# Performance work log

Measured on AMD Instinct MI355X. Metric: run time of the kernel, lower is better.

The kernel has to match this reference:

```python
import jax, jax.numpy as jnp
import numpy as np

D_MODEL = 96
D_INNER = 192   # ssm_ratio * d_model
R = 6           # dt_rank = ceil(96/16)
DH = 32         # d_inner // dt_rank (per-head dim)
K = 4           # scan directions
N = 16          # d_state
EPS = 1e-5


def setup_inputs() -> dict:
    key = jax.random.key(0)
    ks = jax.random.split(key, 10)
    B, H, W = 8, 64, 64
    f = lambda k, s, sc: jax.random.normal(k, s, jnp.float32) * sc
    return dict(
        x=jax.random.normal(ks[0], (B, H, W, D_MODEL), jnp.float32),
        w_in=f(ks[1], (D_MODEL, D_INNER), 0.02),
        w_conv=f(ks[2], (3, 3, 1, D_INNER), 0.1),      # depthwise HWIO
        b_conv=f(ks[3], (D_INNER,), 0.1),
        x_proj_weight=f(ks[4], (K, R + 2 * N, D_INNER), 0.02),
        A_logs=f(ks[5], (K, R), 0.5),
        Ds=jnp.ones((K, R, DH), jnp.float32),
        dt_bias=0.1 * jax.random.uniform(ks[6], (K, R), jnp.float32),
        ln_g=jnp.ones((D_INNER,), jnp.float32),
        ln_b=jnp.zeros((D_INNER,), jnp.float32),
        w_out=f(ks[7], (D_INNER, D_MODEL), 0.02),
    )


def _cross_scan(x):
    # x: (B,H,W,C) -> (B,L,4,C): [row-major, col-major, rev row, rev col]
    B, H, W, C = x.shape
    x0 = x.reshape(B, H * W, C)
    x1 = jnp.transpose(x, (0, 2, 1, 3)).reshape(B, H * W, C)
    return jnp.stack([x0, x1, x0[:, ::-1], x1[:, ::-1]], axis=2)


def _cross_merge(ys, H, W):
    # ys: (B,L,4,C) -> (B,L,C) summed after undoing each scan order
    B, L, _, C = ys.shape
    y_row = ys[:, :, 0] + ys[:, :, 2][:, ::-1]
    y_col = ys[:, :, 1] + ys[:, :, 3][:, ::-1]
    y_col = jnp.transpose(y_col.reshape(B, W, H, C), (0, 2, 1, 3)).reshape(B, L, C)
    return y_row + y_col


def _selective_scan(us, dts, As, Bs, Cs, Dsr, dtb):
    # us:(B,L,KR,DH) dts:(B,L,KR) As:(KR,) Bs,Cs:(B,L,K,N) Dsr:(KR,DH) dtb:(KR,)
    dt = jax.nn.softplus(dts + dtb)                 # (B,L,KR)
    decay = jnp.exp(dt * As)                        # (B,L,KR)
    xu = dt[..., None] * us                         # (B,L,KR,DH)
    Bh = jnp.repeat(Bs, R, axis=2)                  # (B,L,KR,N) head h -> group h//R
    Ch = jnp.repeat(Cs, R, axis=2)
    B_, L, KR, _ = us.shape
    tfirst = lambda a: jnp.moveaxis(a, 1, 0)

    def step(h, inp):
        dec, xu_t, b_t, c_t = inp                   # (B,KR),(B,KR,DH),(B,KR,N),(B,KR,N)
        h = dec[:, :, None, None] * h + xu_t[..., None] * b_t[:, :, None, :]
        y = jnp.einsum('bkdn,bkn->bkd', h, c_t)
        return h, y

    h0 = jnp.zeros((B_, KR, DH, N), us.dtype)
    _, ys = jax.lax.scan(step, h0, (tfirst(decay), tfirst(xu), tfirst(Bh), tfirst(Ch)))
    ys = jnp.moveaxis(ys, 0, 1)                     # (B,L,KR,DH)
    return ys + us * Dsr                            # skip term D*u


def reference(x, w_in, w_conv, b_conv, x_proj_weight, A_logs, Ds, dt_bias, ln_g, ln_b, w_out):
    B, H, W, _ = x.shape
    L = H * W
    xi = x @ w_in                                   # in_proj (no bias)
    xi = jax.lax.conv_general_dilated(
        xi, w_conv, (1, 1), 'SAME', feature_group_count=D_INNER,
        dimension_numbers=('NHWC', 'HWIO', 'NHWC')) + b_conv
    xi = jax.nn.silu(xi)
    xs = _cross_scan(xi)                            # (B,L,4,D_INNER)
    x_dbl = jnp.einsum('blkd,kcd->blkc', xs, x_proj_weight)
    dts = x_dbl[..., :R].reshape(B, L, K * R)
    Bs = x_dbl[..., R:R + N]                        # (B,L,K,N)
    Cs = x_dbl[..., R + N:]
    us = xs.reshape(B, L, K * R, DH)
    As = -jnp.exp(A_logs.astype(jnp.float32)).reshape(K * R)
    Dsr = Ds.reshape(K * R, DH)
    dtb = dt_bias.reshape(K * R)
    ys = _selective_scan(us, dts, As, Bs, Cs, Dsr, dtb)   # (B,L,KR,DH)
    y = _cross_merge(ys.reshape(B, L, K, R * DH), H, W)   # (B,L,D_INNER)
    mu = y.mean(-1, keepdims=True)
    var = ((y - mu) ** 2).mean(-1, keepdims=True)
    y = (y - mu) / jnp.sqrt(var + EPS) * ln_g + ln_b
    y = y.reshape(B, H, W, D_INNER)
    return y @ w_out                                # out_proj (no bias)
```

## Files before the change

### kernel.cpp

```cpp
#include <hip/hip_runtime.h>
#include <hip/hip_bf16.h>

#define BB 8
#define LL 4096
#define DM 96
#define DI 192
#define RRR 6
#define DHH 32
#define KKK 4
#define NNN 16
#define KRR 24
#define NCH 64
#define TT 64
#define RST 48

typedef unsigned short u16;
typedef __attribute__((ext_vector_type(8))) __bf16 bf16x8;
typedef __attribute__((ext_vector_type(4))) float f32x4;

__device__ __forceinline__ float softplus_f(float x){
    float ax = fabsf(x);
    return fmaxf(x, 0.f) + __logf(1.f + __expf(-ax));
}
__device__ __forceinline__ float silu_f(float x){ return x / (1.f + __expf(-x)); }

__device__ __forceinline__ void split_bf16(float v, u16& h, u16& l){
    __bf16 hb = (__bf16)v;
    h = __builtin_bit_cast(u16, hb);
    float r = v - (float)hb;
    l = __builtin_bit_cast(u16, (__bf16)r);
}

__global__ void k0p(const float* __restrict__ W, const float* __restrict__ g,
                    const float* __restrict__ bta, const float* __restrict__ w_out,
                    u16* __restrict__ WhB, u16* __restrict__ WlB,
                    float* __restrict__ wg, float* __restrict__ sgbw){
    int i = blockIdx.x * 256 + threadIdx.x;
    if (i < 2 * 80 * 192){
        int k = i % 192; int n80 = i / 192; int z = n80 / 80; int n = n80 % 80;
        int sub = n / 40, nc = n % 40;
        int dir = (z == 0) ? (sub ? 2 : 0) : (sub ? 3 : 1);
        float v = 0.f;
        if (nc < 6) v = W[(dir * 38 + nc) * DI + k];
        else if (nc >= 8) v = W[(dir * 38 + (nc - 2)) * DI + k];
        u16 h, l; split_bf16(v, h, l);
        WhB[i] = h; WlB[i] = l;
    } else if (i < 30720 + DI * DM){
        int j = i - 30720; int c = j / DM;
        wg[j] = w_out[j] * g[c];
    } else if (i < 30720 + DI * DM + DM){
        int m = i - (30720 + DI * DM);
        float s = 0.f, t = 0.f;
        for (int c = 0; c < DI; ++c){
            float w = w_out[c * DM + m];
            s = fmaf(g[c], w, s);
            t = fmaf(bta[c], w, t);
        }
        sgbw[m] = s; sgbw[DM + m] = t;
    }
}

__global__ __launch_bounds__(384) void k1_inproj(const float* __restrict__ x,
                                                 const float* __restrict__ w_in,
                                                 float* __restrict__ xw){
    __shared__ float xT[DM][36];
    int pix0 = blockIdx.x * 32;
    for (int i = threadIdx.x; i < 32 * 24; i += 384){
        int c4 = i % 24, p = i / 24;
        float4 v = *(const float4*)(x + (size_t)(pix0 + p) * DM + c4 * 4);
        xT[c4 * 4 + 0][p] = v.x; xT[c4 * 4 + 1][p] = v.y;
        xT[c4 * 4 + 2][p] = v.z; xT[c4 * 4 + 3][p] = v.w;
    }
    __syncthreads();
    int cg = threadIdx.x % 48, pg = threadIdx.x / 48;
    int p0 = pg * 4;
    float4 acc[4];
    #pragma unroll
    for (int i = 0; i < 4; ++i) acc[i] = make_float4(0.f, 0.f, 0.f, 0.f);
    const float* wcol = w_in + cg * 4;
    for (int d0 = 0; d0 < DM; d0 += 8){
        float4 wv[8], xv[8];
        #pragma unroll
        for (int j = 0; j < 8; ++j){
            wv[j] = *(const float4*)(wcol + (d0 + j) * DI);
            xv[j] = *(const float4*)(&xT[d0 + j][p0]);
        }
        #pragma unroll
        for (int j = 0; j < 8; ++j){
            float xs[4] = {xv[j].x, xv[j].y, xv[j].z, xv[j].w};
            #pragma unroll
            for (int pi = 0; pi < 4; ++pi){
                acc[pi].x = fmaf(xs[pi], wv[j].x, acc[pi].x);
                acc[pi].y = fmaf(xs[pi], wv[j].y, acc[pi].y);
                acc[pi].z = fmaf(xs[pi], wv[j].z, acc[pi].z);
                acc[pi].w = fmaf(xs[pi], wv[j].w, acc[pi].w);
            }
        }
    }
    #pragma unroll
    for (int pi = 0; pi < 4; ++pi)
        *(float4*)(xw + (size_t)(pix0 + p0 + pi) * DI + cg * 4) = acc[pi];
}

__global__ void k2_conv(const float* __restrict__ xw, const float* __restrict__ wc,
                        const float* __restrict__ bc, float* __restrict__ xi,
                        float* __restrict__ xiT){
    int gid = blockIdx.x * 256 + threadIdx.x;
    int c4 = gid % 48; int pix = gid / 48;
    int b = pix >> 12; int l = pix & 4095; int h = l >> 6; int w = l & 63;
    int c = c4 * 4;
    float4 acc = *(const float4*)(bc + c);
    #pragma unroll
    for (int dh = 0; dh < 3; ++dh){
        int hh = h + dh - 1; if ((unsigned)hh >= 64u) continue;
        #pragma unroll
        for (int dw = 0; dw < 3; ++dw){
            int ww2 = w + dw - 1; if ((unsigned)ww2 >= 64u) continue;
            float4 tap = *(const float4*)(xw + (size_t)((b << 12) + (hh << 6) + ww2) * DI + c);
            float4 wv  = *(const float4*)(wc + (dh * 3 + dw) * DI + c);
            acc.x = fmaf(tap.x, wv.x, acc.x);
            acc.y = fmaf(tap.y, wv.y, acc.y);
            acc.z = fmaf(tap.z, wv.z, acc.z);
            acc.w = fmaf(tap.w, wv.w, acc.w);
        }
    }
    acc.x = silu_f(acc.x); acc.y = silu_f(acc.y); acc.z = silu_f(acc.z); acc.w = silu_f(acc.w);
    *(float4*)(xi + (size_t)pix * DI + c) = acc;
    int lT = ((l & 63) << 6) | (l >> 6);
    *(float4*)(xiT + (size_t)((b << 12) + lT) * DI + c) = acc;
}

__global__ __launch_bounds__(256) void k3seq(const float* __restrict__ xi,
                                             const float* __restrict__ xiT,
                                             const u16* __restrict__ WhB,
                                             const u16* __restrict__ WlB,
                                             const float* __restrict__ A_logs,
                                             const float* __restrict__ dtb,
                                             float* __restrict__ rec){
    __shared__ u16 Xh[64][104];
    __shared__ u16 Xl[64][104];
    int z = blockIdx.y, b = blockIdx.z;
    int l0 = blockIdx.x * 64;
    const float* src = (z ? xiT : xi) + ((((size_t)b) << 12) + l0) * DI;
    int wv = threadIdx.x >> 6, lane = threadIdx.x & 63;
    int quad = lane >> 4, mi = lane & 15;
    int m0 = wv * 16;
    f32x4 acc[5];
    #pragma unroll
    for (int nt = 0; nt < 5; ++nt) acc[nt] = (f32x4){0.f, 0.f, 0.f, 0.f};
    const u16* wh = WhB + (size_t)z * 80 * 192;
    const u16* wl = WlB + (size_t)z * 80 * 192;
    #pragma unroll
    for (int half = 0; half < 2; ++half){
        __syncthreads();
        for (int i = threadIdx.x; i < 1536; i += 256){
            int c4 = i % 24, p = i / 24;
            float4 v = *(const float4*)(src + (size_t)p * DI + half * 96 + c4 * 4);
            u16 h0, h1, h2, h3, q0, q1, q2, q3;
            split_bf16(v.x, h0, q0); split_bf16(v.y, h1, q1);
            split_bf16(v.z, h2, q2); split_bf16(v.w, h3, q3);
            *(ushort4*)&Xh[p][c4 * 4] = make_ushort4(h0, h1, h2, h3);
            *(ushort4*)&Xl[p][c4 * 4] = make_ushort4(q0, q1, q2, q3);
        }
        __syncthreads();
        #pragma unroll
        for (int kt = 0; kt < 3; ++kt){
            int ko = kt * 32 + quad * 8;
            bf16x8 ah = *(const bf16x8*)&Xh[m0 + mi][ko];
            bf16x8 al = *(const bf16x8*)&Xl[m0 + mi][ko];
            int kg = half * 96 + ko;
            #pragma unroll
            for (int nt = 0; nt < 5; ++nt){
                const size_t woff = (size_t)(nt * 16 + mi) * 192 + kg;
                bf16x8 bh = *(const bf16x8*)(wh + woff);
                bf16x8 bl = *(const bf16x8*)(wl + woff);
                acc[nt] = __builtin_amdgcn_mfma_f32_16x16x32_bf16(ah, bh, acc[nt], 0, 0, 0);
                acc[nt] = __builtin_amdgcn_mfma_f32_16x16x32_bf16(al, bh, acc[nt], 0, 0, 0);
                acc[nt] = __builtin_amdgcn_mfma_f32_16x16x32_bf16(ah, bl, acc[nt], 0, 0, 0);
            }
        }
    }
    #pragma unroll
    for (int nt = 0; nt < 5; ++nt){
        int nc = nt * 16 + mi;
        int sub = nc / 40;
        int dir = (z == 0) ? (sub ? 2 : 0) : (sub ? 3 : 1);
        int c40 = nc % 40;
        float* rb = rec + (size_t)(b * KKK + dir) * LL * RST;
        bool isdt = (c40 < 6);
        bool ispad = (c40 == 6) | (c40 == 7);
        float Ac = 0.f, bc = 0.f;
        if (isdt){ Ac = -__expf(A_logs[dir * RRR + c40]); bc = dtb[dir * RRR + c40]; }
        #pragma unroll
        for (int i = 0; i < 4; ++i){
            int l = l0 + m0 + quad * 4 + i;
            int t = (sub == 0) ? l : (LL - 1 - l);
            float v = acc[nt][i];
            float* rw = rb + (size_t)t * RST;
            if (isdt){
                float dt = softplus_f(v + bc);
                rw[c40] = dt;
                rw[c40 + 8] = __expf(dt * Ac);
            } else if (!ispad){
                rw[c40 + 8] = v;
            }
        }
    }
}

__global__ __launch_bounds__(192) void k4a(const float* __restrict__ xi, const float* __restrict__ xiT,
                                           const float* __restrict__ rec, const float* __restrict__ Ds,
                                           float* __restrict__ Pb, float* __restrict__ Sb,
                                           float* __restrict__ pp, __hip_bfloat16* __restrict__ ybuf){
    int chunk = blockIdx.x, k = blockIdx.y, b = blockIdx.z;
    int r = threadIdx.x >> 5, d = threadIdx.x & 31;
    int kr = k * RRR + r;
    float Dv = Ds[kr * DHH + d];
    const float* rp = rec + ((size_t)(b * KKK + k) * LL + chunk * TT) * RST;
    const float* xb = ((k & 1) ? xiT : xi) + (((size_t)b) << 12) * DI + r * DHH + d;
    const float* up; ptrdiff_t ust;
    if (k < 2){ up = xb + (size_t)(chunk * TT) * DI;          ust = DI;  }
    else      { up = xb + (size_t)(LL - 1 - chunk * TT) * DI; ust = -(ptrdiff_t)DI; }
    __hip_bfloat16* yp = ybuf + ((size_t)(k * BB + b) * LL + chunk * TT) * DI + r * DHH + d;
    float* ppp = pp + ((size_t)(b * KKK + k) * RRR + r) * LL + chunk * TT;
    float h[NNN];
    #pragma unroll
    for (int n = 0; n < NNN; ++n) h[n] = 0.f;
    float ppv = 1.f;
    #pragma unroll 2
    for (int tt = 0; tt < TT; ++tt){
        float dt  = rp[r];
        float dec = rp[8 + r];
        float u = *up;
        float xu = dt * u;
        ppv *= dec;
        float Bv[NNN], Cv[NNN];
        *(float4*)(Bv + 0)  = *(const float4*)(rp + 16);
        *(float4*)(Bv + 4)  = *(const float4*)(rp + 20);
        *(float4*)(Bv + 8)  = *(const float4*)(rp + 24);
        *(float4*)(Bv + 12) = *(const float4*)(rp + 28);
        *(float4*)(Cv + 0)  = *(const float4*)(rp + 32);
        *(float4*)(Cv + 4)  = *(const float4*)(rp + 36);
        *(float4*)(Cv + 8)  = *(const float4*)(rp + 40);
        *(float4*)(Cv + 12) = *(const float4*)(rp + 44);
        float y = 0.f;
        #pragma unroll
        for (int n = 0; n < NNN; ++n){
            h[n] = fmaf(dec, h[n], xu * Bv[n]);
            y = fmaf(h[n], Cv[n], y);
        }
        y = fmaf(u, Dv, y);
        *yp = __float2bfloat16(y);
        if (d == 0) ppp[tt] = ppv;
        rp += RST; up += ust; yp += DI;
    }
    size_t sb = (((size_t)(b * KRR + kr) * NCH + chunk) * DHH + d) * NNN;
    #pragma unroll
    for (int n = 0; n < NNN; ++n) Sb[sb + n] = h[n];
    if (d == 0) Pb[(size_t)(b * KRR + kr) * NCH + chunk] = ppv;
}

__global__ __launch_bounds__(256) void k4b(const float* __restrict__ Pb, float* __restrict__ Sb){
    int scan = blockIdx.x >> 1;
    int half = blockIdx.x & 1;
    int tid = half * 256 + threadIdx.x;
    size_t base = (size_t)scan * NCH * 512 + tid;
    const float* Pp = Pb + (size_t)scan * NCH;
    float s[NCH];
    #pragma unroll
    for (int c = 0; c < NCH; ++c) s[c] = Sb[base + (size_t)c * 512];
    float hb = 0.f;
    #pragma unroll
    for (int c = 0; c < NCH; ++c){
        float nv = fmaf(Pp[c], hb, s[c]);
        Sb[base + (size_t)c * 512] = hb;
        hb = nv;
    }
}

__global__ __launch_bounds__(192) void k4corr(const float* __restrict__ rec,
                                              const float* __restrict__ Sb,
                                              const float* __restrict__ pp,
                                              __hip_bfloat16* __restrict__ ybuf){
    int chunk = blockIdx.x + 1;
    int k = blockIdx.y, b = blockIdx.z;
    int r = threadIdx.x >> 5, d = threadIdx.x & 31;
    int kr = k * RRR + r;
    float hi[NNN];
    size_t sb = (((size_t)(b * KRR + kr) * NCH + chunk) * DHH + d) * NNN;
    #pragma unroll
    for (int n = 0; n < NNN; ++n) hi[n] = Sb[sb + n];
    const float* rp = rec + ((size_t)(b * KKK + k) * LL + chunk * TT) * RST + 32;
    const float* ppp = pp + ((size_t)(b * KKK + k) * RRR + r) * LL + chunk * TT;
    __hip_bfloat16* yp = ybuf + ((size_t)(k * BB + b) * LL + chunk * TT) * DI + r * DHH + d;
    #pragma unroll 4
    for (int tt = 0; tt < TT; ++tt){
        float Cv[NNN];
        *(float4*)(Cv + 0)  = *(const float4*)(rp + 0);
        *(float4*)(Cv + 4)  = *(const float4*)(rp + 4);
        *(float4*)(Cv + 8)  = *(const float4*)(rp + 8);
        *(float4*)(Cv + 12) = *(const float4*)(rp + 12);
        float dv = 0.f;
        #pragma unroll
        for (int n = 0; n < NNN; ++n) dv = fmaf(hi[n], Cv[n], dv);
        float y = __bfloat162float(*yp);
        y = fmaf(ppp[tt], dv, y);
        *yp = __float2bfloat16(y);
        rp += RST; yp += DI;
    }
}

__global__ __launch_bounds__(256) void k5_out(const __hip_bfloat16* __restrict__ ybuf,
                       const float* __restrict__ wg, const float* __restrict__ sgbw,
                       float* __restrict__ out){
    __shared__ float yT[DI][36];
    __shared__ float rsL[32], rmL[32];
    int pix0 = blockIdx.x * 32;
    int b = pix0 >> 12;
    int l0 = pix0 & 4095;
    const __hip_bfloat16* y0 = ybuf + (size_t)(0 * BB + b) * LL * DI;
    const __hip_bfloat16* y1 = ybuf + (size_t)(1 * BB + b) * LL * DI;
    const __hip_bfloat16* y2 = ybuf + (size_t)(2 * BB + b) * LL * DI;
    const __hip_bfloat16* y3 = ybuf + (size_t)(3 * BB + b) * LL * DI;
    for (int i = threadIdx.x; i < 32 * DI; i += 256){
        int c = i % DI, p = i / DI;
        int l = l0 + p; int hh = l >> 6, ww = l & 63;
        int lT = (ww << 6) | hh;
        float s = __bfloat162float(y0[(size_t)l * DI + c])
                + __bfloat162float(y2[(size_t)(LL - 1 - l) * DI + c])
                + __bfloat162float(y1[(size_t)lT * DI + c])
                + __bfloat162float(y3[(size_t)(LL - 1 - lT) * DI + c]);
        yT[c][p] = s;
    }
    __syncthreads();
    {
        int p = threadIdx.x >> 3, cg = threadIdx.x & 7;
        float s = 0.f, s2 = 0.f;
        for (int c = cg; c < DI; c += 8){ float v = yT[c][p]; s += v; s2 = fmaf(v, v, s2); }
        s += __shfl_xor(s, 1, 64); s2 += __shfl_xor(s2, 1, 64);
        s += __shfl_xor(s, 2, 64); s2 += __shfl_xor(s2, 2, 64);
        s += __shfl_xor(s, 4, 64); s2 += __shfl_xor(s2, 4, 64);
        if (cg == 0){
            float mu = s * (1.f / DI);
            float var = s2 * (1.f / DI) - mu * mu;
            float rs = rsqrtf(var + 1e-5f);
            rsL[p] = rs; rmL[p] = rs * mu;
        }
    }
    __syncthreads();
    if (threadIdx.x < 192){
        int mg = threadIdx.x % 24, pg = threadIdx.x / 24;
        int p0 = pg * 4;
        float4 acc[4];
        #pragma unroll
        for (int i = 0; i < 4; ++i) acc[i] = make_float4(0.f, 0.f, 0.f, 0.f);
        const float* wcol = wg + mg * 4;
        for (int c0 = 0; c0 < DI; c0 += 8){
            float4 wv[8], yv[8];
            #pragma unroll
            for (int j = 0; j < 8; ++j){
                wv[j] = *(const float4*)(wcol + (c0 + j) * DM);
                yv[j] = *(const float4*)(&yT[c0 + j][p0]);
            }
            #pragma unroll
            for (int j = 0; j < 8; ++j){
                float ys[4] = {yv[j].x, yv[j].y, yv[j].z, yv[j].w};
                #pragma unroll
                for (int pi = 0; pi < 4; ++pi){
                    acc[pi].x = fmaf(ys[pi], wv[j].x, acc[pi].x);
                    acc[pi].y = fmaf(ys[pi], wv[j].y, acc[pi].y);
                    acc[pi].z = fmaf(ys[pi], wv[j].z, acc[pi].z);
                    acc[pi].w = fmaf(ys[pi], wv[j].w, acc[pi].w);
                }
            }
        }
        float4 sg4 = *(const float4*)(sgbw + mg * 4);
        float4 bw4 = *(const float4*)(sgbw + DM + mg * 4);
        #pragma unroll
        for (int pi = 0; pi < 4; ++pi){
            float rs = rsL[p0 + pi], rm = rmL[p0 + pi];
            float4 o;
            o.x = fmaf(acc[pi].x, rs, fmaf(-rm, sg4.x, bw4.x));
            o.y = fmaf(acc[pi].y, rs, fmaf(-rm, sg4.y, bw4.y));
            o.z = fmaf(acc[pi].z, rs, fmaf(-rm, sg4.z, bw4.z));
            o.w = fmaf(acc[pi].w, rs, fmaf(-rm, sg4.w, bw4.w));
            *(float4*)(out + (size_t)(pix0 + p0 + pi) * DM + mg * 4) = o;
        }
    }
}

extern "C" void kernel_launch(void* const* d_in, const int* in_sizes, int n_in,
                              void* d_out, int out_size, void* d_ws, size_t ws_size,
                              hipStream_t stream){
    const float* x      = (const float*)d_in[0];
    const float* w_in   = (const float*)d_in[1];
    const float* w_conv = (const float*)d_in[2];
    const float* b_conv = (const float*)d_in[3];
    const float* xproj  = (const float*)d_in[4];
    const float* A_logs = (const float*)d_in[5];
    const float* Ds     = (const float*)d_in[6];
    const float* dtbias = (const float*)d_in[7];
    const float* ln_g   = (const float*)d_in[8];
    const float* ln_b   = (const float*)d_in[9];
    const float* w_out  = (const float*)d_in[10];
    float* out = (float*)d_out;

    float* ws   = (float*)d_ws;
    float* xi   = ws;
    float* xiT  = xi + 6291456;
    float* Sb   = xiT + 6291456;
    float* Pb   = Sb + 6291456;
    float* pp   = Pb + 16384;
    float* wbase= pp + 786432;
    u16*   WhB  = (u16*)wbase;
    u16*   WlB  = (u16*)(wbase + 15360);
    float* wg   = wbase + 30720;
    float* sgbw = wg + 18432;
    float* big  = sgbw + 192;
    float* xw   = big;
    float* rec  = big;
    __hip_bfloat16* ybuf = (__hip_bfloat16*)(big + 6291456);

    k0p<<<193, 256, 0, stream>>>(xproj, ln_g, ln_b, w_out, WhB, WlB, wg, sgbw);
    k1_inproj<<<1024, 384, 0, stream>>>(x, w_in, xw);
    k2_conv<<<6144, 256, 0, stream>>>(xw, w_conv, b_conv, xi, xiT);
    k3seq<<<dim3(64, 2, BB), 256, 0, stream>>>(xi, xiT, WhB, WlB, A_logs, dtbias, rec);
    k4a<<<dim3(NCH, KKK, BB), 192, 0, stream>>>(xi, xiT, rec, Ds, Pb, Sb, pp, ybuf);
    k4b<<<384, 256, 0, stream>>>(Pb, Sb);
    k4corr<<<dim3(NCH - 1, KKK, BB), 192, 0, stream>>>(rec, Sb, pp, ybuf);
    k5_out<<<1024, 256, 0, stream>>>(ybuf, wg, sgbw, out);
}
```

Before: 279.4 us.

## Halve scan chunk count and software-prefetch next-step inputs in scan kernels

Chunk length for the chunked selective scan doubles to 128 (32 chunks), which halves the state carry buffers and the inter-chunk prefix scan in k4b. The per-step loads of dt, decay, u, B and C in k4a, and of C and the decay prefix in k4corr, are now software-prefetched one step ahead to hide memory latency in the serial recurrence. In exchange, each k4a block runs a longer serial chain and only half as many blocks are launched (1024 instead of 2048), which lowers parallelism on a large GPU. Register pressure also rises from the doubled prefetch set.

```diff
diff --git a/kernel.cpp b/kernel.cpp
--- a/kernel.cpp
+++ b/kernel.cpp
@@ -10,8 +10,8 @@
 #define KKK 4
 #define NNN 16
 #define KRR 24
-#define NCH 64
-#define TT 64
+#define NC2 32
+#define TT2 128
 #define RST 48
 
 typedef unsigned short u16;
@@ -216,33 +216,28 @@
     int r = threadIdx.x >> 5, d = threadIdx.x & 31;
     int kr = k * RRR + r;
     float Dv = Ds[kr * DHH + d];
-    const float* rp = rec + ((size_t)(b * KKK + k) * LL + chunk * TT) * RST;
+    const float* rp = rec + ((size_t)(b * KKK + k) * LL + chunk * TT2) * RST;
     const float* xb = ((k & 1) ? xiT : xi) + (((size_t)b) << 12) * DI + r * DHH + d;
     const float* up; ptrdiff_t ust;
-    if (k < 2){ up = xb + (size_t)(chunk * TT) * DI;          ust = DI;  }
-    else      { up = xb + (size_t)(LL - 1 - chunk * TT) * DI; ust = -(ptrdiff_t)DI; }
-    __hip_bfloat16* yp = ybuf + ((size_t)(k * BB + b) * LL + chunk * TT) * DI + r * DHH + d;
-    float* ppp = pp + ((size_t)(b * KKK + k) * RRR + r) * LL + chunk * TT;
+    if (k < 2){ up = xb + (size_t)(chunk * TT2) * DI;          ust = DI;  }
+    else      { up = xb + (size_t)(LL - 1 - chunk * TT2) * DI; ust = -(ptrdiff_t)DI; }
+    __hip_bfloat16* yp = ybuf + ((size_t)(k * BB + b) * LL + chunk * TT2) * DI + r * DHH + d;
+    float* ppp = pp + ((size_t)(b * KKK + k) * RRR + r) * LL + chunk * TT2;
     float h[NNN];
     #pragma unroll
     for (int n = 0; n < NNN; ++n) h[n] = 0.f;
     float ppv = 1.f;
-    #pragma unroll 2
-    for (int tt = 0; tt < TT; ++tt){
-        float dt  = rp[r];
-        float dec = rp[8 + r];
-        float u = *up;
+
+    auto step = [&](float dt, float dec, float u,
+                    float4 B0, float4 B1, float4 B2, float4 B3,
+                    float4 C0, float4 C1, float4 C2, float4 C3, int tt){
         float xu = dt * u;
         ppv *= dec;
         float Bv[NNN], Cv[NNN];
-        *(float4*)(Bv + 0)  = *(const float4*)(rp + 16);
-        *(float4*)(Bv + 4)  = *(const float4*)(rp + 20);
-        *(float4*)(Bv + 8)  = *(const float4*)(rp + 24);
-        *(float4*)(Bv + 12) = *(const float4*)(rp + 28);
-        *(float4*)(Cv + 0)  = *(const float4*)(rp + 32);
-        *(float4*)(Cv + 4)  = *(const float4*)(rp + 36);
-        *(float4*)(Cv + 8)  = *(const float4*)(rp + 40);
-        *(float4*)(Cv + 12) = *(const float4*)(rp + 44);
+        *(float4*)(Bv + 0) = B0;  *(float4*)(Bv + 4) = B1;
+        *(float4*)(Bv + 8) = B2;  *(float4*)(Bv + 12) = B3;
+        *(float4*)(Cv + 0) = C0;  *(float4*)(Cv + 4) = C1;
+        *(float4*)(Cv + 8) = C2;  *(float4*)(Cv + 12) = C3;
         float y = 0.f;
         #pragma unroll
         for (int n = 0; n < NNN; ++n){
@@ -252,26 +247,48 @@
         y = fmaf(u, Dv, y);
         *yp = __float2bfloat16(y);
         if (d == 0) ppp[tt] = ppv;
-        rp += RST; up += ust; yp += DI;
-    }
-    size_t sb = (((size_t)(b * KRR + kr) * NCH + chunk) * DHH + d) * NNN;
+        yp += DI;
+    };
+
+    float dtc = rp[r], decc = rp[8 + r], uc = *up;
+    float4 B0c = *(const float4*)(rp + 16), B1c = *(const float4*)(rp + 20);
+    float4 B2c = *(const float4*)(rp + 24), B3c = *(const float4*)(rp + 28);
+    float4 C0c = *(const float4*)(rp + 32), C1c = *(const float4*)(rp + 36);
+    float4 C2c = *(const float4*)(rp + 40), C3c = *(const float4*)(rp + 44);
+    for (int tt = 0; tt < TT2 - 1; ++tt){
+        const float* rpn = rp + RST;
+        const float* upn = up + ust;
+        float dtn = rpn[r], decn = rpn[8 + r], un = *upn;
+        float4 B0n = *(const float4*)(rpn + 16), B1n = *(const float4*)(rpn + 20);
+        float4 B2n = *(const float4*)(rpn + 24), B3n = *(const float4*)(rpn + 28);
+        float4 C0n = *(const float4*)(rpn + 32), C1n = *(const float4*)(rpn + 36);
+        float4 C2n = *(const float4*)(rpn + 40), C3n = *(const float4*)(rpn + 44);
+        step(dtc, decc, uc, B0c, B1c, B2c, B3c, C0c, C1c, C2c, C3c, tt);
+        dtc = dtn; decc = decn; uc = un;
+        B0c = B0n; B1c = B1n; B2c = B2n; B3c = B3n;
+        C0c = C0n; C1c = C1n; C2c = C2n; C3c = C3n;
+        rp = rpn; up = upn;
+    }
+    step(dtc, decc, uc, B0c, B1c, B2c, B3c, C0c, C1c, C2c, C3c, TT2 - 1);
+
+    size_t sb = (((size_t)(b * KRR + kr) * NC2 + chunk) * DHH + d) * NNN;
     #pragma unroll
     for (int n = 0; n < NNN; ++n) Sb[sb + n] = h[n];
-    if (d == 0) Pb[(size_t)(b * KRR + kr) * NCH + chunk] = ppv;
+    if (d == 0) Pb[(size_t)(b * KRR + kr) * NC2 + chunk] = ppv;
 }
 
 __global__ __launch_bounds__(256) void k4b(const float* __restrict__ Pb, float* __restrict__ Sb){
     int scan = blockIdx.x >> 1;
     int half = blockIdx.x & 1;
     int tid = half * 256 + threadIdx.x;
-    size_t base = (size_t)scan * NCH * 512 + tid;
-    const float* Pp = Pb + (size_t)scan * NCH;
-    float s[NCH];
-    #pragma unroll
-    for (int c = 0; c < NCH; ++c) s[c] = Sb[base + (size_t)c * 512];
+    size_t base = (size_t)scan * NC2 * 512 + tid;
+    const float* Pp = Pb + (size_t)scan * NC2;
+    float s[NC2];
+    #pragma unroll
+    for (int c = 0; c < NC2; ++c) s[c] = Sb[base + (size_t)c * 512];
     float hb = 0.f;
     #pragma unroll
-    for (int c = 0; c < NCH; ++c){
+    for (int c = 0; c < NC2; ++c){
         float nv = fmaf(Pp[c], hb, s[c]);
         Sb[base + (size_t)c * 512] = hb;
         hb = nv;
@@ -287,26 +304,36 @@
     int r = threadIdx.x >> 5, d = threadIdx.x & 31;
     int kr = k * RRR + r;
     float hi[NNN];
-    size_t sb = (((size_t)(b * KRR + kr) * NCH + chunk) * DHH + d) * NNN;
+    size_t sb = (((size_t)(b * KRR + kr) * NC2 + chunk) * DHH + d) * NNN;
     #pragma unroll
     for (int n = 0; n < NNN; ++n) hi[n] = Sb[sb + n];
-    const float* rp = rec + ((size_t)(b * KKK + k) * LL + chunk * TT) * RST + 32;
-    const float* ppp = pp + ((size_t)(b * KKK + k) * RRR + r) * LL + chunk * TT;
-    __hip_bfloat16* yp = ybuf + ((size_t)(k * BB + b) * LL + chunk * TT) * DI + r * DHH + d;
-    #pragma unroll 4
-    for (int tt = 0; tt < TT; ++tt){
+    const float* rp = rec + ((size_t)(b * KKK + k) * LL + chunk * TT2) * RST + 32;
+    const float* ppp = pp + ((size_t)(b * KKK + k) * RRR + r) * LL + chunk * TT2;
+    __hip_bfloat16* yp = ybuf + ((size_t)(k * BB + b) * LL + chunk * TT2) * DI + r * DHH + d;
+
+    float4 C0c = *(const float4*)(rp + 0), C1c = *(const float4*)(rp + 4);
+    float4 C2c = *(const float4*)(rp + 8), C3c = *(const float4*)(rp + 12);
+    float ppc = ppp[0];
+    for (int tt = 0; tt < TT2; ++tt){
+        float4 C0n, C1n, C2n, C3n; float ppn = 0.f;
+        if (tt < TT2 - 1){
+            const float* rpn = rp + RST;
+            C0n = *(const float4*)(rpn + 0); C1n = *(const float4*)(rpn + 4);
+            C2n = *(const float4*)(rpn + 8); C3n = *(const float4*)(rpn + 12);
+            ppn = ppp[tt + 1];
+            rp = rpn;
+        }
         float Cv[NNN];
-        *(float4*)(Cv + 0)  = *(const float4*)(rp + 0);
-        *(float4*)(Cv + 4)  = *(const float4*)(rp + 4);
-        *(float4*)(Cv + 8)  = *(const float4*)(rp + 8);
-        *(float4*)(Cv + 12) = *(const float4*)(rp + 12);
+        *(float4*)(Cv + 0) = C0c; *(float4*)(Cv + 4) = C1c;
+        *(float4*)(Cv + 8) = C2c; *(float4*)(Cv + 12) = C3c;
         float dv = 0.f;
         #pragma unroll
         for (int n = 0; n < NNN; ++n) dv = fmaf(hi[n], Cv[n], dv);
         float y = __bfloat162float(*yp);
-        y = fmaf(ppp[tt], dv, y);
+        y = fmaf(ppc, dv, y);
         *yp = __float2bfloat16(y);
-        rp += RST; yp += DI;
+        yp += DI;
+        C0c = C0n; C1c = C1n; C2c = C2n; C3c = C3n; ppc = ppn;
     }
 }
 
@@ -409,8 +436,8 @@
     float* xi   = ws;
     float* xiT  = xi + 6291456;
     float* Sb   = xiT + 6291456;
-    float* Pb   = Sb + 6291456;
-    float* pp   = Pb + 16384;
+    float* Pb   = Sb + 3145728;
+    float* pp   = Pb + 6144;
     float* wbase= pp + 786432;
     u16*   WhB  = (u16*)wbase;
     u16*   WlB  = (u16*)(wbase + 15360);
@@ -425,8 +452,8 @@
     k1_inproj<<<1024, 384, 0, stream>>>(x, w_in, xw);
     k2_conv<<<6144, 256, 0, stream>>>(xw, w_conv, b_conv, xi, xiT);
     k3seq<<<dim3(64, 2, BB), 256, 0, stream>>>(xi, xiT, WhB, WlB, A_logs, dtbias, rec);
-    k4a<<<dim3(NCH, KKK, BB), 192, 0, stream>>>(xi, xiT, rec, Ds, Pb, Sb, pp, ybuf);
+    k4a<<<dim3(NC2, KKK, BB), 192, 0, stream>>>(xi, xiT, rec, Ds, Pb, Sb, pp, ybuf);
     k4b<<<384, 256, 0, stream>>>(Pb, Sb);
-    k4corr<<<dim3(NCH - 1, KKK, BB), 192, 0, stream>>>(rec, Sb, pp, ybuf);
+    k4corr<<<dim3(NC2 - 1, KKK, BB), 192, 0, stream>>>(rec, Sb, pp, ybuf);
     k5_out<<<1024, 256, 0, stream>>>(ybuf, wg, sgbw, out);
 }
```

Measured after the change: 308.0 us. +10.2%, slower.
